# Optimization experiments

Measured on AMD Instinct MI355X. Metric: run time of the kernel, lower is better.

Reference implementation:

```python
import jax, jax.numpy as jnp
import numpy as np

EPS = 1e-5
K = 5

def _bn(x, g, b):
    # BatchNorm1d in training mode: biased batch statistics
    mu = jnp.mean(x, axis=0)
    var = jnp.mean((x - mu) ** 2, axis=0)
    return (x - mu) * jax.lax.rsqrt(var + EPS) * g + b

def setup_inputs():
    key = jax.random.key(0)
    ks = jax.random.split(key, 16)
    N, M, D, F = 16384, 8192, 512, 2048
    s = 0.02
    return dict(
        src=jax.random.normal(ks[0], (N, D), jnp.float32),
        anchor_2=jax.random.normal(ks[1], (M, D), jnp.float32),
        W_dim=jax.random.normal(ks[2], (D, D), jnp.float32) * s,
        b_dim=jnp.zeros((D,), jnp.float32),
        W_fus=jax.random.normal(ks[3], (2 * D, D), jnp.float32) * s,
        b_fus=jnp.zeros((D,), jnp.float32),
        W_e1=jax.random.normal(ks[4], (D, F), jnp.float32) * s,
        b_e1=jnp.zeros((F,), jnp.float32),
        W_e2=jax.random.normal(ks[5], (F, D), jnp.float32) * s,
        b_e2=jnp.zeros((D,), jnp.float32),
        g1=jnp.ones((D,), jnp.float32), bt1=jnp.zeros((D,), jnp.float32),
        g2=jnp.ones((D,), jnp.float32), bt2=jnp.zeros((D,), jnp.float32),
        W_d=jax.random.normal(ks[6], (D, D), jnp.float32) * s,
        b_d=jnp.zeros((D,), jnp.float32),
        g_d=jnp.ones((D,), jnp.float32), bt_d=jnp.zeros((D,), jnp.float32),
    )

def reference(src, anchor_2, W_dim, b_dim, W_fus, b_fus, W_e1, b_e1, W_e2, b_e2,
              g1, bt1, g2, bt2, W_d, b_d, g_d, bt_d):
    # kNN in Euclidean metric (sklearn NearestNeighbors): squared distances suffice
    # d2[n,m] = ||src_n||^2 - 2 src_n . a_m + ||a_m||^2   -> [N, M]
    d2 = (jnp.sum(src * src, axis=1, keepdims=True)
          - 2.0 * (src @ anchor_2.T)
          + jnp.sum(anchor_2 * anchor_2, axis=1)[None, :])
    _, idx = jax.lax.top_k(-d2, K)                      # [N, K] nearest anchors
    neigh = jnp.mean(anchor_2[idx], axis=1)             # gather + mean -> [N, D]
    a_map = neigh @ W_dim + b_dim                       # linear_dim
    comb = jnp.concatenate([src, a_map], axis=1) @ W_fus + b_fus
    comb = _bn(comb, g1, bt1)                           # norm1
    # encoder MLP (dropout is identity in eval)
    t = jnp.tanh(comb @ W_e1 + b_e1) @ W_e2 + b_e2
    comb = _bn(comb + t, g2, bt2)                       # residual + norm2
    out = jnp.tanh(_bn(comb @ W_d + b_d, g_d, bt_d))    # decoder
    return out
```

## Files before the change

kernel.cpp:

```cpp
#include <hip/hip_runtime.h>
#include <math.h>

#define N_ROWS 16384
#define M_ANCH 8192
#define DDIM   512
#define FDIM   2048
#define KNN    5
#define BN_EPS 1e-5f
#define CHUNK  8192
#define SEED   1024
#define CAND_MAX 256
#define MARGIN 6.0f
#define QSCALE 28.0f
#define TWO_INV_S2 (2.0f / (QSCALE * QSCALE))

typedef _Float16 f16;
typedef _Float16 f16x8 __attribute__((ext_vector_type(8)));
typedef _Float16 f16x4 __attribute__((ext_vector_type(4)));
typedef float f32x4 __attribute__((ext_vector_type(4)));
typedef int   i32x4 __attribute__((ext_vector_type(4)));

__device__ __forceinline__ void async_copy16(const void* g, void* l) {
    __builtin_amdgcn_global_load_lds(
        (const __attribute__((address_space(1))) void*)g,
        (__attribute__((address_space(3))) void*)l, 16, 0, 0);
}

__device__ __forceinline__ bool kless(float k1, int i1, float k2, int i2) {
    return (k1 < k2) || (k1 == k2 && i1 < i2);
}

__device__ __forceinline__ void insert5(float (&bk)[KNN], int (&bi)[KNN], float key, int id) {
    if (!kless(key, id, bk[4], bi[4])) return;
    bool c3 = kless(key, id, bk[3], bi[3]);
    bool c2 = kless(key, id, bk[2], bi[2]);
    bool c1 = kless(key, id, bk[1], bi[1]);
    bool c0 = kless(key, id, bk[0], bi[0]);
    bk[4] = c3 ? bk[3] : key;                  bi[4] = c3 ? bi[3] : id;
    bk[3] = c3 ? (c2 ? bk[2] : key) : bk[3];   bi[3] = c3 ? (c2 ? bi[2] : id) : bi[3];
    bk[2] = c2 ? (c1 ? bk[1] : key) : bk[2];   bi[2] = c2 ? (c1 ? bi[1] : id) : bi[2];
    bk[1] = c1 ? (c0 ? bk[0] : key) : bk[1];   bi[1] = c1 ? (c0 ? bi[0] : id) : bi[1];
    bk[0] = c0 ? key : bk[0];                  bi[0] = c0 ? id : bi[0];
}

__global__ void zero_kernel(float* p, int n) {
    int i = blockIdx.x * blockDim.x + threadIdx.x;
    if (i < n) p[i] = 0.f;
}

__global__ __launch_bounds__(256) void quant_i8_kernel(const float* __restrict__ X,
                                                       unsigned int* __restrict__ Y, int n4) {
    int i = blockIdx.x * 256 + threadIdx.x;
    if (i >= n4) return;
    float4 v = ((const float4*)X)[i];
    int a = (int)rintf(v.x * QSCALE); a = a > 127 ? 127 : (a < -127 ? -127 : a);
    int b = (int)rintf(v.y * QSCALE); b = b > 127 ? 127 : (b < -127 ? -127 : b);
    int c = (int)rintf(v.z * QSCALE); c = c > 127 ? 127 : (c < -127 ? -127 : c);
    int d = (int)rintf(v.w * QSCALE); d = d > 127 ? 127 : (d < -127 ? -127 : d);
    Y[i] = (unsigned int)(a & 255) | ((unsigned int)(b & 255) << 8)
         | ((unsigned int)(c & 255) << 16) | ((unsigned int)(d & 255) << 24);
}

__global__ __launch_bounds__(256) void anchor_norm_kernel(const float* __restrict__ a,
                                                          float* __restrict__ norm_a) {
    int wave = threadIdx.x >> 6, lane = threadIdx.x & 63;
    int row = blockIdx.x * 4 + wave;
    const float4* ar = (const float4*)(a + (size_t)row * DDIM);
    float4 v1 = ar[lane * 2];
    float4 v2 = ar[lane * 2 + 1];
    float s = v1.x*v1.x + v1.y*v1.y + v1.z*v1.z + v1.w*v1.w
            + v2.x*v2.x + v2.y*v2.y + v2.z*v2.z + v2.w*v2.w;
    for (int off = 32; off; off >>= 1) s += __shfl_xor(s, off, 64);
    if (lane == 0) norm_a[row] = s;
}

template<int COLLECT>
__global__ __launch_bounds__(256) void gemm_i8(
    const char* __restrict__ A, const char* __restrict__ B,
    const float* __restrict__ norm, const float* __restrict__ thr,
    int* __restrict__ cnt, int* __restrict__ cand_i, int idofs,
    float* __restrict__ C, int Ncols)
{
    __shared__ char As[2][128 * 64];
    __shared__ char Bs[2][128 * 64];
    const int t = threadIdx.x;
    const int w = t >> 6, l = t & 63;
    const int m0 = blockIdx.y * 128, n0 = blockIdx.x * 128;
    const int wm = (w & 1) * 64, wn = (w >> 1) * 64;

    i32x4 acc[4][4];
    #pragma unroll
    for (int i = 0; i < 4; ++i)
        #pragma unroll
        for (int j = 0; j < 4; ++j) acc[i][j] = (i32x4){0, 0, 0, 0};

    const int srow = l >> 2;
    const int gq = ((l & 3) - (srow >> 1)) & 3;
    const int skoff = gq * 16;
    const int sqf = (((l >> 4) + (((l & 15) >> 1) & 3)) & 3) * 16;

    auto STAGE = [&](int buf, int kt) {
        int k0 = kt * 64;
        #pragma unroll
        for (int s = 0; s < 2; ++s) {
            int grp = w * 2 + s;
            int row = grp * 16 + srow;
            async_copy16(A + (size_t)(m0 + row) * DDIM + k0 + skoff,
                         &As[buf][grp * 1024 + l * 16]);
            async_copy16(B + (size_t)(n0 + row) * DDIM + k0 + skoff,
                         &Bs[buf][grp * 1024 + l * 16]);
        }
    };

    STAGE(0, 0);
    __syncthreads();

    for (int kt = 0; kt < 8; ++kt) {
        int cur = kt & 1;
        if (kt < 7) STAGE(cur ^ 1, kt + 1);
        i32x4 af[4], bf[4];
        #pragma unroll
        for (int i = 0; i < 4; ++i)
            af[i] = *(const i32x4*)&As[cur][(wm + i * 16 + (l & 15)) * 64 + sqf];
        #pragma unroll
        for (int j = 0; j < 4; ++j)
            bf[j] = *(const i32x4*)&Bs[cur][(wn + j * 16 + (l & 15)) * 64 + sqf];
        #pragma unroll
        for (int i = 0; i < 4; ++i)
            #pragma unroll
            for (int j = 0; j < 4; ++j)
                acc[i][j] = __builtin_amdgcn_mfma_i32_16x16x64_i8(af[i], bf[j], acc[i][j], 0, 0, 0);
        __syncthreads();
    }

    float nj[4];
    #pragma unroll
    for (int j = 0; j < 4; ++j) nj[j] = norm[n0 + wn + j * 16 + (l & 15)];

    if (COLLECT) {
        float thr4[4][4];
        #pragma unroll
        for (int i = 0; i < 4; ++i) {
            float4 tv = *(const float4*)&thr[m0 + wm + i * 16 + (l >> 4) * 4];
            thr4[i][0] = tv.x; thr4[i][1] = tv.y; thr4[i][2] = tv.z; thr4[i][3] = tv.w;
        }
        #pragma unroll
        for (int i = 0; i < 4; ++i)
            #pragma unroll
            for (int j = 0; j < 4; ++j)
                #pragma unroll
                for (int r = 0; r < 4; ++r) {
                    float key = nj[j] - TWO_INV_S2 * (float)acc[i][j][r];
                    if (key < thr4[i][r]) {
                        int row = m0 + wm + i * 16 + (l >> 4) * 4 + r;
                        int pos = atomicAdd(&cnt[row], 1);
                        if (pos < CAND_MAX)
                            cand_i[(size_t)row * CAND_MAX + pos] =
                                idofs + n0 + wn + j * 16 + (l & 15);
                    }
                }
    } else {
        #pragma unroll
        for (int i = 0; i < 4; ++i)
            #pragma unroll
            for (int j = 0; j < 4; ++j)
                #pragma unroll
                for (int r = 0; r < 4; ++r) {
                    int m = m0 + wm + i * 16 + (l >> 4) * 4 + r;
                    int n = n0 + wn + j * 16 + (l & 15);
                    C[(size_t)m * Ncols + n] = nj[j] - TWO_INV_S2 * (float)acc[i][j][r];
                }
    }
}

__global__ __launch_bounds__(256) void topk_scan_kernel(
    const float* __restrict__ g, float* __restrict__ thrbuf,
    int* __restrict__ cnt, int* __restrict__ cand_i)
{
    int row = blockIdx.x * 4 + (threadIdx.x >> 6);
    int lane = threadIdx.x & 63;
    const float* grow = g + (size_t)row * SEED;
    float4 v0 = *(const float4*)(grow + lane * 4);
    float4 v1 = *(const float4*)(grow + 256 + lane * 4);
    float4 v2 = *(const float4*)(grow + 512 + lane * 4);
    float4 v3 = *(const float4*)(grow + 768 + lane * 4);
    float bk[KNN]; int bi[KNN];
    #pragma unroll
    for (int q = 0; q < KNN; ++q) { bk[q] = 3.0e38f; bi[q] = 0x7fffffff; }
    int c = lane * 4;
    insert5(bk, bi, v0.x, c);       insert5(bk, bi, v0.y, c + 1);
    insert5(bk, bi, v0.z, c + 2);   insert5(bk, bi, v0.w, c + 3);
    insert5(bk, bi, v1.x, c + 256); insert5(bk, bi, v1.y, c + 257);
    insert5(bk, bi, v1.z, c + 258); insert5(bk, bi, v1.w, c + 259);
    insert5(bk, bi, v2.x, c + 512); insert5(bk, bi, v2.y, c + 513);
    insert5(bk, bi, v2.z, c + 514); insert5(bk, bi, v2.w, c + 515);
    insert5(bk, bi, v3.x, c + 768); insert5(bk, bi, v3.y, c + 769);
    insert5(bk, bi, v3.z, c + 770); insert5(bk, bi, v3.w, c + 771);
    for (int off = 32; off >= 1; off >>= 1) {
        float ok[KNN]; int oi[KNN];
        #pragma unroll
        for (int q = 0; q < KNN; ++q) {
            ok[q] = __shfl_xor(bk[q], off, 64);
            oi[q] = __shfl_xor(bi[q], off, 64);
        }
        #pragma unroll
        for (int q = 0; q < KNN; ++q) insert5(bk, bi, ok[q], oi[q]);
    }
    float thr = bk[4] + MARGIN;
    if (lane == 0) thrbuf[row] = thr;
    int* rci = cand_i + (size_t)row * CAND_MAX;
    #define PUSH(v, id) if ((v) < thr) { int pos = atomicAdd(&cnt[row], 1); \
                                         if (pos < CAND_MAX) rci[pos] = (id); }
    PUSH(v0.x, c)       PUSH(v0.y, c + 1)   PUSH(v0.z, c + 2)   PUSH(v0.w, c + 3)
    PUSH(v1.x, c + 256) PUSH(v1.y, c + 257) PUSH(v1.z, c + 258) PUSH(v1.w, c + 259)
    PUSH(v2.x, c + 512) PUSH(v2.y, c + 513) PUSH(v2.z, c + 514) PUSH(v2.w, c + 515)
    PUSH(v3.x, c + 768) PUSH(v3.y, c + 769) PUSH(v3.z, c + 770) PUSH(v3.w, c + 771)
    #undef PUSH
}

__global__ __launch_bounds__(256) void rescore_kernel(
    const float* __restrict__ src, const float* __restrict__ anchor,
    const float* __restrict__ norm_a, const int* __restrict__ cnt,
    const int* __restrict__ cand_i, int* __restrict__ bi_state)
{
    int row = blockIdx.x * 4 + (threadIdx.x >> 6);
    int lane = threadIdx.x & 63;
    const float4* sp = (const float4*)(src + (size_t)row * DDIM);
    float4 s0 = sp[lane * 2], s1 = sp[lane * 2 + 1];
    float bk[KNN]; int bi[KNN];
    #pragma unroll
    for (int q = 0; q < KNN; ++q) { bk[q] = 3.0e38f; bi[q] = 0x7fffffff; }
    int c = cnt[row]; if (c > CAND_MAX) c = CAND_MAX;
    const int* ci = cand_i + (size_t)row * CAND_MAX;
    for (int p = 0; p < c; ++p) {
        int id = ci[p];
        const float4* ap = (const float4*)(anchor + (size_t)id * DDIM);
        float4 a0 = ap[lane * 2], a1 = ap[lane * 2 + 1];
        float d = s0.x*a0.x + s0.y*a0.y + s0.z*a0.z + s0.w*a0.w
                + s1.x*a1.x + s1.y*a1.y + s1.z*a1.z + s1.w*a1.w;
        #pragma unroll
        for (int off = 32; off; off >>= 1) d += __shfl_xor(d, off, 64);
        float key = norm_a[id] - 2.f * d;
        insert5(bk, bi, key, id);
    }
    if (lane == 0) {
        #pragma unroll
        for (int q = 0; q < KNN; ++q) bi_state[row * KNN + q] = bi[q];
    }
}

__global__ __launch_bounds__(256) void gather_mean_kernel(
    const float* __restrict__ anchor, const int* __restrict__ bi_state,
    float* __restrict__ neigh)
{
    int row = blockIdx.x * 4 + (threadIdx.x >> 6);
    int lane = threadIdx.x & 63;
    const int* bi = bi_state + row * KNN;
    int i0 = bi[0], i1 = bi[1], i2 = bi[2], i3 = bi[3], i4 = bi[4];
    const float4* a0 = (const float4*)(anchor + (size_t)i0 * DDIM);
    const float4* a1 = (const float4*)(anchor + (size_t)i1 * DDIM);
    const float4* a2 = (const float4*)(anchor + (size_t)i2 * DDIM);
    const float4* a3 = (const float4*)(anchor + (size_t)i3 * DDIM);
    const float4* a4 = (const float4*)(anchor + (size_t)i4 * DDIM);
    float4* np = (float4*)(neigh + (size_t)row * DDIM);
    #pragma unroll
    for (int p = 0; p < 2; ++p) {
        int c4 = lane + 64 * p;
        float4 v0 = a0[c4], v1 = a1[c4], v2 = a2[c4], v3 = a3[c4], v4 = a4[c4];
        float4 o;
        o.x = (v0.x + v1.x + v2.x + v3.x + v4.x) * 0.2f;
        o.y = (v0.y + v1.y + v2.y + v3.y + v4.y) * 0.2f;
        o.z = (v0.z + v1.z + v2.z + v3.z + v4.z) * 0.2f;
        o.w = (v0.w + v1.w + v2.w + v3.w + v4.w) * 0.2f;
        np[c4] = o;
    }
}

template<int ADDC0, int TANH, int K>
__global__ __launch_bounds__(256) void gemm_split_nt(
    const float* __restrict__ A, const f16* __restrict__ Bw,
    const float* __restrict__ bias, const float* __restrict__ C0,
    float* __restrict__ C, int Ncols)
{
    __shared__ f16 Ah[128 * 32];
    __shared__ f16 Al[128 * 32];
    __shared__ f16 Bh[128 * 32];
    __shared__ f16 Bl[128 * 32];
    const int t = threadIdx.x;
    const int w = t >> 6, l = t & 63;
    const int m0 = blockIdx.y * 128, n0 = blockIdx.x * 128;
    const int wm = (w & 1) * 64, wn = (w >> 1) * 64;
    const int K2 = 2 * K;

    f32x4 acc[4][4];
    #pragma unroll
    for (int i = 0; i < 4; ++i)
        #pragma unroll
        for (int j = 0; j < 4; ++j) acc[i][j] = (f32x4){0.f, 0.f, 0.f, 0.f};

    const int ar = t >> 1;
    const int ac = (t & 1) * 16;
    const int arq = (ar >> 1) & 3;
    const int s0 = (((t & 1) * 2 + 0 + arq) & 3) * 8;
    const int s1 = (((t & 1) * 2 + 1 + arq) & 3) * 8;
    const int srow = l >> 2;
    const int gq = ((l & 3) - (srow >> 1)) & 3;
    const int skoff = gq * 8;
    const int sqf = (((l >> 4) + (((l & 15) >> 1) & 3)) & 3) * 8;

    for (int k0 = 0; k0 < K; k0 += 32) {
        __syncthreads();
        #pragma unroll
        for (int s = 0; s < 2; ++s) {
            int grp = w * 2 + s;
            int row = grp * 16 + srow;
            const f16* bp = Bw + (size_t)(n0 + row) * K2 + k0 + skoff;
            async_copy16(bp, Bh + grp * 512 + l * 8);
            async_copy16(bp + K, Bl + grp * 512 + l * 8);
        }
        {
            const float* ap = A + (size_t)(m0 + ar) * K + k0 + ac;
            float xs[16];
            *(float4*)&xs[0]  = *(const float4*)ap;
            *(float4*)&xs[4]  = *(const float4*)(ap + 4);
            *(float4*)&xs[8]  = *(const float4*)(ap + 8);
            *(float4*)&xs[12] = *(const float4*)(ap + 12);
            f16x8 h0, h1, lo0, lo1;
            #pragma unroll
            for (int e = 0; e < 8; ++e) {
                f16 hh = (f16)xs[e];
                h0[e] = hh; lo0[e] = (f16)(xs[e] - (float)hh);
                f16 hh2 = (f16)xs[8 + e];
                h1[e] = hh2; lo1[e] = (f16)(xs[8 + e] - (float)hh2);
            }
            *(f16x8*)&Ah[ar * 32 + s0] = h0;  *(f16x8*)&Ah[ar * 32 + s1] = h1;
            *(f16x8*)&Al[ar * 32 + s0] = lo0; *(f16x8*)&Al[ar * 32 + s1] = lo1;
        }
        __syncthreads();
        f16x8 afh[4], afl[4], bfh[4], bfl[4];
        #pragma unroll
        for (int i = 0; i < 4; ++i) {
            int base = (wm + i * 16 + (l & 15)) * 32 + sqf;
            afh[i] = *(const f16x8*)(Ah + base);
            afl[i] = *(const f16x8*)(Al + base);
        }
        #pragma unroll
        for (int j = 0; j < 4; ++j) {
            int base = (wn + j * 16 + (l & 15)) * 32 + sqf;
            bfh[j] = *(const f16x8*)(Bh + base);
            bfl[j] = *(const f16x8*)(Bl + base);
        }
        #pragma unroll
        for (int i = 0; i < 4; ++i)
            #pragma unroll
            for (int j = 0; j < 4; ++j) {
                acc[i][j] = __builtin_amdgcn_mfma_f32_16x16x32_f16(afh[i], bfh[j], acc[i][j], 0, 0, 0);
                acc[i][j] = __builtin_amdgcn_mfma_f32_16x16x32_f16(afl[i], bfh[j], acc[i][j], 0, 0, 0);
                acc[i][j] = __builtin_amdgcn_mfma_f32_16x16x32_f16(afh[i], bfl[j], acc[i][j], 0, 0, 0);
            }
    }
    float bv[4];
    #pragma unroll
    for (int j = 0; j < 4; ++j)
        bv[j] = bias ? bias[n0 + wn + j * 16 + (l & 15)] : 0.f;
    #pragma unroll
    for (int i = 0; i < 4; ++i)
        #pragma unroll
        for (int j = 0; j < 4; ++j)
            #pragma unroll
            for (int r = 0; r < 4; ++r) {
                int m = m0 + wm + i * 16 + (l >> 4) * 4 + r;
                int n = n0 + wn + j * 16 + (l & 15);
                float v = acc[i][j][r] + bv[j];
                if (ADDC0) v += C0[(size_t)m * Ncols + n];
                if (TANH)  v = tanhf(v);
                C[(size_t)m * Ncols + n] = v;
            }
}

__global__ __launch_bounds__(256) void wsplit_kernel(const float* __restrict__ W,
                                                     f16* __restrict__ Wt,
                                                     int K, int N)
{
    __shared__ float tile[64][65];
    const int t = threadIdx.x;
    const int kb = blockIdx.y * 64, nb = blockIdx.x * 64;
    #pragma unroll
    for (int i = 0; i < 4; ++i) {
        int r = (t >> 4) + i * 16;
        int c = (t & 15) * 4;
        *(float4*)&tile[r][c] = *(const float4*)&W[(size_t)(kb + r) * N + nb + c];
    }
    __syncthreads();
    const int r2 = t >> 2;
    const int kc = (t & 3) * 16;
    f16x8 h0, h1, lo0, lo1;
    #pragma unroll
    for (int e = 0; e < 8; ++e) {
        float x = tile[kc + e][r2];
        f16 hh = (f16)x; h0[e] = hh; lo0[e] = (f16)(x - (float)hh);
        float y = tile[kc + 8 + e][r2];
        f16 hh2 = (f16)y; h1[e] = hh2; lo1[e] = (f16)(y - (float)hh2);
    }
    f16* base = Wt + (size_t)(nb + r2) * 2 * K + kb + kc;
    *(f16x8*)base = h0; *(f16x8*)(base + 8) = h1;
    *(f16x8*)(base + K) = lo0; *(f16x8*)(base + K + 8) = lo1;
}

__global__ __launch_bounds__(256) void bcomb_kernel(const float* __restrict__ b_dim,
                                                    const float* __restrict__ W_fus2,
                                                    const float* __restrict__ b_fus,
                                                    float* __restrict__ b_comb)
{
    int n = blockIdx.x * 256 + threadIdx.x;
    if (n >= DDIM) return;
    float s = b_fus[n];
    for (int k = 0; k < DDIM; ++k) s += b_dim[k] * W_fus2[(size_t)k * DDIM + n];
    b_comb[n] = s;
}

template<int ACT>
__global__ __launch_bounds__(256) void gemm_kernel(
    const float* __restrict__ A, int K1,
    const float* __restrict__ A2, int K2,
    const float* __restrict__ B, const float* __restrict__ bias,
    float* __restrict__ C, int Ncols)
{
    __shared__ float As[16][132];
    __shared__ float Bs[16][128];
    const int t = threadIdx.x;
    const int n0 = blockIdx.x * 128;
    const int m0 = blockIdx.y * 128;
    const int ty = t >> 4, tx = t & 15;
    const int K = K1 + K2;

    float acc[8][8];
    #pragma unroll
    for (int i = 0; i < 8; ++i)
        #pragma unroll
        for (int j = 0; j < 8; ++j) acc[i][j] = 0.f;

    const int ar = t >> 1;
    const int akc = (t & 1) * 8;
    const int bkr = t >> 4;
    const int bc = (t & 15) * 8;

    for (int k0 = 0; k0 < K; k0 += 16) {
        int kk = k0 + akc;
        float4 v0, v1;
        if (kk < K1) {
            const float* p = A + (size_t)(m0 + ar) * K1 + kk;
            v0 = *(const float4*)p; v1 = *(const float4*)(p + 4);
        } else {
            const float* p = A2 + (size_t)(m0 + ar) * K2 + (kk - K1);
            v0 = *(const float4*)p; v1 = *(const float4*)(p + 4);
        }
        const float* bp = B + (size_t)(k0 + bkr) * Ncols + n0 + bc;
        float4 w0 = *(const float4*)bp, w1 = *(const float4*)(bp + 4);
        __syncthreads();
        As[akc+0][ar] = v0.x; As[akc+1][ar] = v0.y; As[akc+2][ar] = v0.z; As[akc+3][ar] = v0.w;
        As[akc+4][ar] = v1.x; As[akc+5][ar] = v1.y; As[akc+6][ar] = v1.z; As[akc+7][ar] = v1.w;
        *(float4*)&Bs[bkr][bc] = w0; *(float4*)&Bs[bkr][bc + 4] = w1;
        __syncthreads();
        #pragma unroll
        for (int k = 0; k < 16; ++k) {
            float a[8], b[8];
            *(float4*)&a[0] = *(const float4*)&As[k][ty * 8];
            *(float4*)&a[4] = *(const float4*)&As[k][ty * 8 + 4];
            *(float4*)&b[0] = *(const float4*)&Bs[k][tx * 4];
            *(float4*)&b[4] = *(const float4*)&Bs[k][64 + tx * 4];
            #pragma unroll
            for (int i = 0; i < 8; ++i)
                #pragma unroll
                for (int j = 0; j < 8; ++j) acc[i][j] += a[i] * b[j];
        }
    }
    float4 bv0 = *(const float4*)(bias + n0 + tx * 4);
    float4 bv1 = *(const float4*)(bias + n0 + 64 + tx * 4);
    #pragma unroll
    for (int i = 0; i < 8; ++i) {
        int row = m0 + ty * 8 + i;
        float4 o0, o1;
        o0.x = acc[i][0] + bv0.x; o0.y = acc[i][1] + bv0.y;
        o0.z = acc[i][2] + bv0.z; o0.w = acc[i][3] + bv0.w;
        o1.x = acc[i][4] + bv1.x; o1.y = acc[i][5] + bv1.y;
        o1.z = acc[i][6] + bv1.z; o1.w = acc[i][7] + bv1.w;
        if (ACT == 1) {
            o0.x = tanhf(o0.x); o0.y = tanhf(o0.y); o0.z = tanhf(o0.z); o0.w = tanhf(o0.w);
            o1.x = tanhf(o1.x); o1.y = tanhf(o1.y); o1.z = tanhf(o1.z); o1.w = tanhf(o1.w);
        }
        *(float4*)(C + (size_t)row * Ncols + n0 + tx * 4) = o0;
        *(float4*)(C + (size_t)row * Ncols + n0 + 64 + tx * 4) = o1;
    }
}

__global__ __launch_bounds__(256) void bn_stats_kernel(const float* __restrict__ X,
                                                       float* __restrict__ sums)
{
    __shared__ float red[8][64];
    int lane = threadIdx.x & 63;
    int rl = threadIdx.x >> 6;
    int c = blockIdx.x * 64 + lane;
    int chunk = N_ROWS / gridDim.y;
    int rbeg = blockIdx.y * chunk;
    float s = 0.f, s2 = 0.f;
    for (int r = rbeg + rl; r < rbeg + chunk; r += 4) {
        float v = X[(size_t)r * DDIM + c];
        s += v; s2 += v * v;
    }
    red[rl][lane] = s; red[4 + rl][lane] = s2;
    __syncthreads();
    if (threadIdx.x < 64) {
        float ts = red[0][lane] + red[1][lane] + red[2][lane] + red[3][lane];
        float t2 = red[4][lane] + red[5][lane] + red[6][lane] + red[7][lane];
        atomicAdd(&sums[c], ts);
        atomicAdd(&sums[DDIM + c], t2);
    }
}

template<int TANH>
__global__ __launch_bounds__(256) void bn_apply_kernel(
    const float* __restrict__ X, float* __restrict__ Y,
    const float* __restrict__ sums, const float* __restrict__ g,
    const float* __restrict__ b, float invN)
{
    size_t i = (size_t)blockIdx.x * 256 + threadIdx.x;
    int cg = (int)(i % (DDIM / 4));
    int c = cg * 4;
    float4 x = ((const float4*)X)[i];
    float4 sm = *(const float4*)(sums + c);
    float4 sq = *(const float4*)(sums + DDIM + c);
    float4 gv = *(const float4*)(g + c);
    float4 bv = *(const float4*)(b + c);
    float m, var, rs;
    m = sm.x * invN; var = sq.x * invN - m * m; rs = rsqrtf(var + BN_EPS);
    x.x = (x.x - m) * rs * gv.x + bv.x;
    m = sm.y * invN; var = sq.y * invN - m * m; rs = rsqrtf(var + BN_EPS);
    x.y = (x.y - m) * rs * gv.y + bv.y;
    m = sm.z * invN; var = sq.z * invN - m * m; rs = rsqrtf(var + BN_EPS);
    x.z = (x.z - m) * rs * gv.z + bv.z;
    m = sm.w * invN; var = sq.w * invN - m * m; rs = rsqrtf(var + BN_EPS);
    x.w = (x.w - m) * rs * gv.w + bv.w;
    if (TANH) { x.x = tanhf(x.x); x.y = tanhf(x.y); x.z = tanhf(x.z); x.w = tanhf(x.w); }
    ((float4*)Y)[i] = x;
}

extern "C" void kernel_launch(void* const* d_in, const int* in_sizes, int n_in,
                              void* d_out, int out_size, void* d_ws, size_t ws_size,
                              hipStream_t stream)
{
    const float* src   = (const float*)d_in[0];
    const float* anc   = (const float*)d_in[1];
    const float* W_dim = (const float*)d_in[2];
    const float* b_dim = (const float*)d_in[3];
    const float* W_fus = (const float*)d_in[4];
    const float* b_fus = (const float*)d_in[5];
    const float* W_e1  = (const float*)d_in[6];
    const float* b_e1  = (const float*)d_in[7];
    const float* W_e2  = (const float*)d_in[8];
    const float* b_e2  = (const float*)d_in[9];
    const float* g1    = (const float*)d_in[10];
    const float* bt1   = (const float*)d_in[11];
    const float* g2    = (const float*)d_in[12];
    const float* bt2   = (const float*)d_in[13];
    const float* W_d   = (const float*)d_in[14];
    const float* b_d   = (const float*)d_in[15];
    const float* g_d   = (const float*)d_in[16];
    const float* bt_d  = (const float*)d_in[17];
    float* out = (float*)d_out;

    float* ws = (float*)d_ws;
    float* score  = ws;
    float* bufA   = ws + 16777216;
    char*  src2q  = (char*)(ws + 25165824);
    char*  anc2q  = (char*)(ws + 37748736);
    f16*   wbase  = (f16*)(ws + 25165824);
    f16*   Wt_fus1  = wbase;
    f16*   Wt_comb2 = wbase + 524288;
    f16*   Wt_e1    = wbase + 1048576;
    f16*   Wt_e2    = wbase + 3145728;
    f16*   Wt_d     = wbase + 5242880;
    float* W_comb2  = ws + 44040192;
    float* norm_a   = ws + 44302336;
    float* sums1    = ws + 44310528;
    float* sums2    = sums1 + 1024;
    float* sums3    = sums2 + 1024;
    float* zeros512 = ws + 44313600;
    float* b_comb   = ws + 44314112;
    int*   bi_state = (int*)(ws + 44396544);
    float* thrbuf   = ws + 44478464;
    int*   cnt      = (int*)(ws + 44494848);
    int*   cand_i   = (int*)(ws + 48705536);

    const float invN = 1.0f / (float)N_ROWS;
    float* hbuf = score;

    zero_kernel<<<dim3(14), 256, 0, stream>>>(sums1, 3584);
    zero_kernel<<<dim3(64), 256, 0, stream>>>((float*)cnt, 16384);
    quant_i8_kernel<<<dim3(N_ROWS * DDIM / 1024), 256, 0, stream>>>(
        src, (unsigned int*)src2q, N_ROWS * DDIM / 4);
    quant_i8_kernel<<<dim3(M_ANCH * DDIM / 1024), 256, 0, stream>>>(
        anc, (unsigned int*)anc2q, M_ANCH * DDIM / 4);
    anchor_norm_kernel<<<dim3(M_ANCH / 4), 256, 0, stream>>>(anc, norm_a);

    gemm_i8<0><<<dim3(SEED / 128, N_ROWS / 128), 256, 0, stream>>>(
        src2q, anc2q, norm_a, nullptr, nullptr, nullptr, 0, score, SEED);
    topk_scan_kernel<<<dim3(N_ROWS / 4), 256, 0, stream>>>(
        score, thrbuf, cnt, cand_i);
    gemm_i8<1><<<dim3((M_ANCH - SEED) / 128, N_ROWS / 128), 256, 0, stream>>>(
        src2q, anc2q + (size_t)SEED * DDIM, norm_a + SEED, thrbuf,
        cnt, cand_i, SEED, nullptr, 0);
    rescore_kernel<<<dim3(N_ROWS / 4), 256, 0, stream>>>(
        src, anc, norm_a, cnt, cand_i, bi_state);
    gather_mean_kernel<<<dim3(N_ROWS / 4), 256, 0, stream>>>(anc, bi_state, bufA);

    wsplit_kernel<<<dim3(DDIM / 64, DDIM / 64), 256, 0, stream>>>(W_fus, Wt_fus1, DDIM, DDIM);
    wsplit_kernel<<<dim3(FDIM / 64, DDIM / 64), 256, 0, stream>>>(W_e1, Wt_e1, DDIM, FDIM);
    wsplit_kernel<<<dim3(DDIM / 64, FDIM / 64), 256, 0, stream>>>(W_e2, Wt_e2, FDIM, DDIM);
    wsplit_kernel<<<dim3(DDIM / 64, DDIM / 64), 256, 0, stream>>>(W_d, Wt_d, DDIM, DDIM);
    gemm_kernel<0><<<dim3(4, 4), 256, 0, stream>>>(
        W_dim, DDIM, nullptr, 0, W_fus + DDIM * DDIM, zeros512, W_comb2, DDIM);
    bcomb_kernel<<<dim3(2), 256, 0, stream>>>(b_dim, W_fus + DDIM * DDIM, b_fus, b_comb);
    wsplit_kernel<<<dim3(DDIM / 64, DDIM / 64), 256, 0, stream>>>(W_comb2, Wt_comb2, DDIM, DDIM);

    gemm_split_nt<0, 0, DDIM><<<dim3(DDIM / 128, N_ROWS / 128), 256, 0, stream>>>(
        src, Wt_fus1, b_comb, nullptr, out, DDIM);
    gemm_split_nt<1, 0, DDIM><<<dim3(DDIM / 128, N_ROWS / 128), 256, 0, stream>>>(
        bufA, Wt_comb2, nullptr, out, out, DDIM);
    bn_stats_kernel<<<dim3(DDIM / 64, 16), 256, 0, stream>>>(out, sums1);
    bn_apply_kernel<0><<<dim3(8192), 256, 0, stream>>>(out, out, sums1, g1, bt1, invN);

    for (int r0 = 0; r0 < N_ROWS; r0 += CHUNK) {
        gemm_split_nt<0, 1, DDIM><<<dim3(FDIM / 128, CHUNK / 128), 256, 0, stream>>>(
            out + (size_t)r0 * DDIM, Wt_e1, b_e1, nullptr, hbuf, FDIM);
        gemm_split_nt<1, 0, FDIM><<<dim3(DDIM / 128, CHUNK / 128), 256, 0, stream>>>(
            hbuf, Wt_e2, b_e2, out + (size_t)r0 * DDIM, bufA + (size_t)r0 * DDIM,
            DDIM);
    }
    bn_stats_kernel<<<dim3(DDIM / 64, 16), 256, 0, stream>>>(bufA, sums2);
    bn_apply_kernel<0><<<dim3(8192), 256, 0, stream>>>(bufA, bufA, sums2, g2, bt2, invN);

    gemm_split_nt<0, 0, DDIM><<<dim3(DDIM / 128, N_ROWS / 128), 256, 0, stream>>>(
        bufA, Wt_d, b_d, nullptr, out, DDIM);
    bn_stats_kernel<<<dim3(DDIM / 64, 16), 256, 0, stream>>>(out, sums3);
    bn_apply_kernel<1><<<dim3(8192), 256, 0, stream>>>(out, out, sums3, g_d, bt_d, invN);
}
```

Baseline: 1.515 ms.

## Prefetch candidate anchor rows into LDS and fuse gather-mean into rescore

The rescore kernel now double-buffers candidate anchor rows into per-wave LDS with async global-to-LDS copies, using a manual vmcnt wait to overlap the next row's load with the current dot product. Candidate norms are stored next to candidate ids when candidates are collected, which removes the dependent norm_a lookup during rescoring. The separate gather_mean kernel and its bi_state round trip are folded into the end of rescore. This adds LDS use and relies on the hand-counted vmcnt value matching the exact order in which loads are issued.

```diff
diff --git a/kernel.cpp b/kernel.cpp
--- a/kernel.cpp
+++ b/kernel.cpp
@@ -78,8 +78,8 @@
 __global__ __launch_bounds__(256) void gemm_i8(
     const char* __restrict__ A, const char* __restrict__ B,
     const float* __restrict__ norm, const float* __restrict__ thr,
-    int* __restrict__ cnt, int* __restrict__ cand_i, int idofs,
-    float* __restrict__ C, int Ncols)
+    int* __restrict__ cnt, int* __restrict__ cand_i, float* __restrict__ cand_n,
+    int idofs, float* __restrict__ C, int Ncols)
 {
     __shared__ char As[2][128 * 64];
     __shared__ char Bs[2][128 * 64];
@@ -154,9 +154,11 @@
                     if (key < thr4[i][r]) {
                         int row = m0 + wm + i * 16 + (l >> 4) * 4 + r;
                         int pos = atomicAdd(&cnt[row], 1);
-                        if (pos < CAND_MAX)
+                        if (pos < CAND_MAX) {
                             cand_i[(size_t)row * CAND_MAX + pos] =
                                 idofs + n0 + wn + j * 16 + (l & 15);
+                            cand_n[(size_t)row * CAND_MAX + pos] = nj[j];
+                        }
                     }
                 }
     } else {
@@ -174,8 +176,9 @@
 }
 
 __global__ __launch_bounds__(256) void topk_scan_kernel(
-    const float* __restrict__ g, float* __restrict__ thrbuf,
-    int* __restrict__ cnt, int* __restrict__ cand_i)
+    const float* __restrict__ g, const float* __restrict__ norm_a,
+    float* __restrict__ thrbuf, int* __restrict__ cnt,
+    int* __restrict__ cand_i, float* __restrict__ cand_n)
 {
     int row = blockIdx.x * 4 + (threadIdx.x >> 6);
     int lane = threadIdx.x & 63;
@@ -209,8 +212,10 @@
     float thr = bk[4] + MARGIN;
     if (lane == 0) thrbuf[row] = thr;
     int* rci = cand_i + (size_t)row * CAND_MAX;
+    float* rcn = cand_n + (size_t)row * CAND_MAX;
     #define PUSH(v, id) if ((v) < thr) { int pos = atomicAdd(&cnt[row], 1); \
-                                         if (pos < CAND_MAX) rci[pos] = (id); }
+                                         if (pos < CAND_MAX) { rci[pos] = (id); \
+                                         rcn[pos] = norm_a[(id)]; } }
     PUSH(v0.x, c)       PUSH(v0.y, c + 1)   PUSH(v0.z, c + 2)   PUSH(v0.w, c + 3)
     PUSH(v1.x, c + 256) PUSH(v1.y, c + 257) PUSH(v1.z, c + 258) PUSH(v1.w, c + 259)
     PUSH(v2.x, c + 512) PUSH(v2.y, c + 513) PUSH(v2.z, c + 514) PUSH(v2.w, c + 515)
@@ -220,48 +225,55 @@
 
 __global__ __launch_bounds__(256) void rescore_kernel(
     const float* __restrict__ src, const float* __restrict__ anchor,
-    const float* __restrict__ norm_a, const int* __restrict__ cnt,
-    const int* __restrict__ cand_i, int* __restrict__ bi_state)
-{
-    int row = blockIdx.x * 4 + (threadIdx.x >> 6);
-    int lane = threadIdx.x & 63;
+    const int* __restrict__ cnt, const int* __restrict__ cand_i,
+    const float* __restrict__ cand_n, float* __restrict__ neigh)
+{
+    __shared__ float lb[4][2][DDIM];
+    int wv = threadIdx.x >> 6, lane = threadIdx.x & 63;
+    int row = blockIdx.x * 4 + wv;
     const float4* sp = (const float4*)(src + (size_t)row * DDIM);
     float4 s0 = sp[lane * 2], s1 = sp[lane * 2 + 1];
-    float bk[KNN]; int bi[KNN];
-    #pragma unroll
-    for (int q = 0; q < KNN; ++q) { bk[q] = 3.0e38f; bi[q] = 0x7fffffff; }
     int c = cnt[row]; if (c > CAND_MAX) c = CAND_MAX;
     const int* ci = cand_i + (size_t)row * CAND_MAX;
+    const float* cn = cand_n + (size_t)row * CAND_MAX;
+
+    float bk[KNN]; int bi[KNN];
+    #pragma unroll
+    for (int q = 0; q < KNN; ++q) { bk[q] = 3.0e38f; bi[q] = 0x7fffffff; }
+
+    auto PREF = [&](int buf, int id) {
+        const float* gp = anchor + (size_t)id * DDIM;
+        async_copy16(gp + lane * 4, &lb[wv][buf][lane * 4]);
+        async_copy16(gp + 256 + lane * 4, &lb[wv][buf][256 + lane * 4]);
+    };
+
+    int   id_c = ci[0];          float n_c = cn[0];
+    int   id_n = ci[1];          float n_n = cn[1];
+    PREF(0, id_c);
+    PREF(1, id_n);
+
     for (int p = 0; p < c; ++p) {
-        int id = ci[p];
-        const float4* ap = (const float4*)(anchor + (size_t)id * DDIM);
-        float4 a0 = ap[lane * 2], a1 = ap[lane * 2 + 1];
+        int id_f = 0; float n_f = 0.f;
+        if (p + 2 < c) { id_f = ci[p + 2]; n_f = cn[p + 2]; }
+        asm volatile("s_waitcnt vmcnt(4)" ::: "memory");
+        const float* bc = &lb[wv][p & 1][0];
+        float4 a0 = *(const float4*)&bc[lane * 8];
+        float4 a1 = *(const float4*)&bc[lane * 8 + 4];
         float d = s0.x*a0.x + s0.y*a0.y + s0.z*a0.z + s0.w*a0.w
                 + s1.x*a1.x + s1.y*a1.y + s1.z*a1.z + s1.w*a1.w;
         #pragma unroll
         for (int off = 32; off; off >>= 1) d += __shfl_xor(d, off, 64);
-        float key = norm_a[id] - 2.f * d;
-        insert5(bk, bi, key, id);
-    }
-    if (lane == 0) {
-        #pragma unroll
-        for (int q = 0; q < KNN; ++q) bi_state[row * KNN + q] = bi[q];
-    }
-}
-
-__global__ __launch_bounds__(256) void gather_mean_kernel(
-    const float* __restrict__ anchor, const int* __restrict__ bi_state,
-    float* __restrict__ neigh)
-{
-    int row = blockIdx.x * 4 + (threadIdx.x >> 6);
-    int lane = threadIdx.x & 63;
-    const int* bi = bi_state + row * KNN;
-    int i0 = bi[0], i1 = bi[1], i2 = bi[2], i3 = bi[3], i4 = bi[4];
-    const float4* a0 = (const float4*)(anchor + (size_t)i0 * DDIM);
-    const float4* a1 = (const float4*)(anchor + (size_t)i1 * DDIM);
-    const float4* a2 = (const float4*)(anchor + (size_t)i2 * DDIM);
-    const float4* a3 = (const float4*)(anchor + (size_t)i3 * DDIM);
-    const float4* a4 = (const float4*)(anchor + (size_t)i4 * DDIM);
+        insert5(bk, bi, n_c - 2.f * d, id_c);
+        if (p + 2 < c) PREF(p & 1, id_f);
+        id_c = id_n; n_c = n_n;
+        id_n = id_f; n_n = n_f;
+    }
+
+    const float4* a0 = (const float4*)(anchor + (size_t)bi[0] * DDIM);
+    const float4* a1 = (const float4*)(anchor + (size_t)bi[1] * DDIM);
+    const float4* a2 = (const float4*)(anchor + (size_t)bi[2] * DDIM);
+    const float4* a3 = (const float4*)(anchor + (size_t)bi[3] * DDIM);
+    const float4* a4 = (const float4*)(anchor + (size_t)bi[4] * DDIM);
     float4* np = (float4*)(neigh + (size_t)row * DDIM);
     #pragma unroll
     for (int p = 0; p < 2; ++p) {
@@ -580,6 +592,7 @@
     f16*   Wt_e1    = wbase + 1048576;
     f16*   Wt_e2    = wbase + 3145728;
     f16*   Wt_d     = wbase + 5242880;
+    float* cand_n   = ws + 29360128;
     float* W_comb2  = ws + 44040192;
     float* norm_a   = ws + 44302336;
     float* sums1    = ws + 44310528;
@@ -587,7 +600,6 @@
     float* sums3    = sums2 + 1024;
     float* zeros512 = ws + 44313600;
     float* b_comb   = ws + 44314112;
-    int*   bi_state = (int*)(ws + 44396544);
     float* thrbuf   = ws + 44478464;
     int*   cnt      = (int*)(ws + 44494848);
     int*   cand_i   = (int*)(ws + 48705536);
@@ -604,15 +616,14 @@
     anchor_norm_kernel<<<dim3(M_ANCH / 4), 256, 0, stream>>>(anc, norm_a);
 
     gemm_i8<0><<<dim3(SEED / 128, N_ROWS / 128), 256, 0, stream>>>(
-        src2q, anc2q, norm_a, nullptr, nullptr, nullptr, 0, score, SEED);
+        src2q, anc2q, norm_a, nullptr, nullptr, nullptr, nullptr, 0, score, SEED);
     topk_scan_kernel<<<dim3(N_ROWS / 4), 256, 0, stream>>>(
-        score, thrbuf, cnt, cand_i);
+        score, norm_a, thrbuf, cnt, cand_i, cand_n);
     gemm_i8<1><<<dim3((M_ANCH - SEED) / 128, N_ROWS / 128), 256, 0, stream>>>(
         src2q, anc2q + (size_t)SEED * DDIM, norm_a + SEED, thrbuf,
-        cnt, cand_i, SEED, nullptr, 0);
+        cnt, cand_i, cand_n, SEED, nullptr, 0);
     rescore_kernel<<<dim3(N_ROWS / 4), 256, 0, stream>>>(
-        src, anc, norm_a, cnt, cand_i, bi_state);
-    gather_mean_kernel<<<dim3(N_ROWS / 4), 256, 0, stream>>>(anc, bi_state, bufA);
+        src, anc, cnt, cand_i, cand_n, bufA);
 
     wsplit_kernel<<<dim3(DDIM / 64, DDIM / 64), 256, 0, stream>>>(W_fus, Wt_fus1, DDIM, DDIM);
     wsplit_kernel<<<dim3(FDIM / 64, DDIM / 64), 256, 0, stream>>>(W_e1, Wt_e1, DDIM, FDIM);
```

Measured after the change: 1.644 ms. +8.6%, slower.
